# Kernel optimization log

Hardware: AMD Instinct MI355X
Metric: run time of the kernel (lower is better)

Reference implementation:

```python
import jax, jax.numpy as jnp
import numpy as np

FEAT_IN = 64     # len(nonterminals)
EMB = 256        # embedding_dim
K = 30           # sortk
B = 48           # batch items
NG = 11          # graphs per item (1 goal + 10 env)
G = B * NG       # 528 graphs
NPG = 192        # nodes per graph
EPG = 384        # edges per graph
N = G * NPG
E = G * EPG
D = 3 * EMB + 1  # 769, concat channel dim = conv5 kernel/stride
DENSE = (K // 2 - 5 + 1) * EMB  # 11*256 = 2816


def setup_inputs() -> dict:
    key = jax.random.key(0)
    ks = jax.random.split(key, 12)
    x = jax.random.normal(ks[0], (N, FEAT_IN), jnp.float32)
    # edges within each graph, no self loops (remove_self_loops in original)
    src_l = jax.random.randint(ks[1], (E,), 0, NPG)
    off = jax.random.randint(ks[2], (E,), 1, NPG)
    dst_l = (src_l + off) % NPG
    goff = (jnp.arange(E) // EPG) * NPG
    src = (src_l + goff).astype(jnp.int32)
    dst = (dst_l + goff).astype(jnp.int32)

    def lin(k, fi, fo):
        return (jax.random.normal(k, (fi, fo), jnp.float32) / np.float32(np.sqrt(fi)))

    return dict(
        x=x, src=src, dst=dst,
        W1=lin(ks[3], FEAT_IN, EMB), b1=jnp.zeros((EMB,), jnp.float32),
        W2=lin(ks[4], EMB, EMB), b2=jnp.zeros((EMB,), jnp.float32),
        W3=lin(ks[5], EMB, EMB), b3=jnp.zeros((EMB,), jnp.float32),
        W4=lin(ks[6], EMB, 1), b4=jnp.zeros((1,), jnp.float32),
        w5=jax.random.normal(ks[7], (EMB // 2, 1, D), jnp.float32) / np.float32(np.sqrt(D)),
        bc5=jnp.zeros((EMB // 2,), jnp.float32),
        w6=jax.random.normal(ks[8], (EMB, EMB // 2, 5), jnp.float32) / np.float32(np.sqrt(5 * EMB // 2)),
        bc6=jnp.zeros((EMB,), jnp.float32),
        Wc1=lin(ks[9], NG * DENSE, EMB), bc1=jnp.zeros((EMB,), jnp.float32),
        Wc2=lin(ks[10], EMB, 10), bc2=jnp.zeros((10,), jnp.float32),
    )


def _gcn(x, W, b, src, dst):
    # PyG GCNConv: add self loops, symmetric norm D^-1/2 (A+I) D^-1/2 (XW) + b
    h = x @ W
    deg = jnp.ones((N,), h.dtype).at[dst].add(1.0)  # +1 for self loop
    dis = jax.lax.rsqrt(deg)
    msg = h[src] * (dis[src] * dis[dst])[:, None]
    agg = jnp.zeros_like(h).at[dst].add(msg)
    return agg + h * (dis * dis)[:, None] + b  # self-loop norm = 1/deg


def _conv1d(x, w, b, stride):
    y = jax.lax.conv_general_dilated(x, w, (stride,), 'VALID',
                                     dimension_numbers=('NCH', 'OIH', 'NCH'))
    return y + b[None, :, None]


def reference(x, src, dst, W1, b1, W2, b2, W3, b3, W4, b4,
              w5, bc5, w6, bc6, Wc1, bc1, Wc2, bc2):
    x1 = jnp.tanh(_gcn(x, W1, b1, src, dst))
    x2 = jnp.tanh(_gcn(x1, W2, b2, src, dst))
    x3 = jnp.tanh(_gcn(x2, W3, b3, src, dst))
    x4 = jnp.tanh(_gcn(x3, W4, b4, src, dst))
    xc = jnp.concatenate([x1, x2, x3, x4], axis=-1)  # [N, D]
    xg = xc.reshape(G, NPG, D)
    # global_sort_pool: sort nodes per graph by last channel (desc), take top K
    _, idx = jax.lax.top_k(xg[:, :, -1], K)          # [G, K]
    xs = jnp.take_along_axis(xg, idx[:, :, None], axis=1)  # [G, K, D]
    seq = xs.reshape(G, 1, K * D)
    y = jax.nn.relu(_conv1d(seq, w5, bc5, D))        # [G, EMB/2, K]
    y = y.reshape(G, EMB // 2, K // 2, 2).max(axis=-1)  # MaxPool1d(2,2)
    y = jax.nn.relu(_conv1d(y, w6, bc6, 1))          # [G, EMB, K//2-4]
    emb = y.reshape(B, NG * DENSE)                   # 11 graphs per item, flattened
    h = jax.nn.relu(emb @ Wc1 + bc1)
    logits = h @ Wc2 + bc2                           # dropout is identity at eval
    return logits
```

## Files before the change

kernel.cpp:

```cpp
#include <hip/hip_runtime.h>
#include <hip/hip_bf16.h>

#define EMB   256
#define KSORT 30
#define BATCH 48
#define NGPI  11
#define GG    528
#define NPG   192
#define EPG   384
#define DCH   769
#define GC    528
#define MC    (GC*NPG)
#define EC    (GC*EPG)
#define FQ    44
#define FCH   (2816/FQ)
#define KB5   5

__device__ __forceinline__ int clampi(int v, int lo, int hi) {
  return v < lo ? lo : (v > hi ? hi : v);
}

__device__ __attribute__((aligned(16))) float g_c1[MC * EMB];
__device__ __attribute__((aligned(16))) float g_c2[MC * EMB];
__device__ __attribute__((aligned(16))) float g_c3[MC * EMB];
__device__ __attribute__((aligned(16))) float g_tb[MC * EMB];
__device__ __attribute__((aligned(16))) float g_dis[MC];
__device__ __attribute__((aligned(16))) float g_s4[MC];
__device__ __attribute__((aligned(16))) float g_x4[MC];
__device__ __attribute__((aligned(16))) int   g_indptr[MC + 1];
__device__ __attribute__((aligned(16))) int   g_ssrc[EC];
__device__ __attribute__((aligned(16))) int   g_idx[GC * KSORT];
__device__ __attribute__((aligned(16))) float g_w5t[DCH * 128];
__device__ __attribute__((aligned(16))) float g_w6t[640 * 256];
__device__ __attribute__((aligned(16))) float g_y[GC * 128 * 30];
__device__ __attribute__((aligned(16))) float g_z[GG * 2816];
__device__ __attribute__((aligned(16))) float g_hp[NGPI * FQ * BATCH * 256];
__device__ __attribute__((aligned(16))) float g_h[BATCH * 256];

__device__ __forceinline__ float* selbuf(int s) {
  return s == 0 ? g_c1 : (s == 1 ? g_c2 : g_c3);
}

__global__ __launch_bounds__(192) void build_csr_k(const int* __restrict__ src,
    const int* __restrict__ dst, int g0) {
  __shared__ int cnt[NPG];
  __shared__ int offs[NPG];
  int g = blockIdx.x, t = threadIdx.x;
  int gg = g0 + g;
  cnt[t] = 0;
  __syncthreads();
  int ebase = gg * EPG, gnb = gg * NPG, lnb = g * NPG;
  for (int e = t; e < EPG; e += 192) {
    int dl = clampi(dst[ebase + e] - gnb, 0, NPG - 1);
    atomicAdd(&cnt[dl], 1);
  }
  __syncthreads();
  if (t == 0) {
    int run = g * EPG;
    for (int i = 0; i < NPG; i++) { offs[i] = run; run += cnt[i]; }
  }
  __syncthreads();
  g_indptr[lnb + t] = offs[t];
  g_dis[lnb + t] = 1.0f / sqrtf(1.0f + (float)cnt[t]);
  if (g == 0 && t == 0) g_indptr[MC] = EC;
  __syncthreads();
  for (int e = t; e < EPG; e += 192) {
    int ee = ebase + e;
    int dl = clampi(dst[ee] - gnb, 0, NPG - 1);
    int pos = clampi(atomicAdd(&offs[dl], 1), 0, EC - 1);
    g_ssrc[pos] = clampi(src[ee] - gnb, 0, NPG - 1) + lnb;
  }
}

template<bool AX>
__global__ __launch_bounds__(256) void gemm_k(const float* __restrict__ Ax,
    int asel, const float* __restrict__ W, int Kd) {
  __shared__ float As[16 * 192];
  __shared__ float Bs[16][68];
  const int m0 = blockIdx.x * 128, n0 = blockIdx.y * 128;
  const int t = threadIdx.x;
  const int tx = t & 15, ty = t >> 4;
  const int arow = t >> 1, acol = (t & 1) * 8;
  const int awr = (arow >> 3) * 12 + (arow & 7);
  const int brow = t >> 4, bcol = tx * 4;
  float acc[8][8];
#pragma unroll
  for (int i = 0; i < 8; i++)
#pragma unroll
    for (int j = 0; j < 8; j++) acc[i][j] = 0.f;
  const float* Ap = AX ? Ax : selbuf(asel);
  const float* arp = Ap + (size_t)(m0 + arow) * Kd + acol;
  const float* bsp = W + (size_t)brow * EMB + n0 + bcol;
  const float* Wg = W + n0 + 64 + tx * 4;
  const int nt = Kd >> 4;
  float4 pa0 = *(const float4*)(arp);
  float4 pa1 = *(const float4*)(arp + 4);
  float4 pb  = *(const float4*)(bsp);
  for (int it = 0; it < nt; ++it) {
    As[(acol + 0) * 192 + awr] = pa0.x;
    As[(acol + 1) * 192 + awr] = pa0.y;
    As[(acol + 2) * 192 + awr] = pa0.z;
    As[(acol + 3) * 192 + awr] = pa0.w;
    As[(acol + 4) * 192 + awr] = pa1.x;
    As[(acol + 5) * 192 + awr] = pa1.y;
    As[(acol + 6) * 192 + awr] = pa1.z;
    As[(acol + 7) * 192 + awr] = pa1.w;
    *(float4*)&Bs[brow][bcol] = pb;
    __syncthreads();
    if (it + 1 < nt) {
      const float* ap = arp + (it + 1) * 16;
      pa0 = *(const float4*)(ap);
      pa1 = *(const float4*)(ap + 4);
      pb  = *(const float4*)(bsp + (size_t)(it + 1) * 16 * EMB);
    }
    const float* Wk = Wg + (size_t)(it * 16) * EMB;
#pragma unroll
    for (int kk = 0; kk < 16; kk++) {
      float a[8], b[8];
      *(float4*)&a[0] = *(const float4*)&As[kk * 192 + ty * 12];
      *(float4*)&a[4] = *(const float4*)&As[kk * 192 + ty * 12 + 4];
      *(float4*)&b[0] = *(const float4*)&Bs[kk][bcol];
      *(float4*)&b[4] = *(const float4*)(Wk + kk * EMB);
#pragma unroll
      for (int i = 0; i < 8; i++)
#pragma unroll
        for (int j = 0; j < 8; j++) acc[i][j] += a[i] * b[j];
    }
    __syncthreads();
  }
#pragma unroll
  for (int i = 0; i < 8; i++) {
    float* cp = g_tb + (size_t)(m0 + ty * 8 + i) * EMB + n0 + tx * 4;
    *(float4*)cp = make_float4(acc[i][0], acc[i][1], acc[i][2], acc[i][3]);
    *(float4*)(cp + 64) = make_float4(acc[i][4], acc[i][5], acc[i][6], acc[i][7]);
  }
}

__global__ __launch_bounds__(256) void agg_k(int osel,
    const float* __restrict__ bias, const float* __restrict__ W4) {
  int nb = (blockIdx.x & 7) * (MC / 4 / 8) + (blockIdx.x >> 3);
  int n = nb * 4 + (threadIdx.x >> 6);
  int lane = threadIdx.x & 63;
  float dn = g_dis[n];
  const float4* H4 = (const float4*)g_tb;
  float4 hv = H4[(size_t)n * 64 + lane];
  float sc = dn * dn;
  float ax = hv.x * sc, ay = hv.y * sc, az = hv.z * sc, aw = hv.w * sc;
  int beg = g_indptr[n], end = g_indptr[n + 1];
  for (int j = beg; j < end; j++) {
    int s = g_ssrc[j];
    float c = g_dis[s] * dn;
    float4 v = H4[(size_t)s * 64 + lane];
    ax += v.x * c; ay += v.y * c; az += v.z * c; aw += v.w * c;
  }
  float4 bv = ((const float4*)bias)[lane];
  float4 o;
  o.x = tanhf(ax + bv.x);
  o.y = tanhf(ay + bv.y);
  o.z = tanhf(az + bv.z);
  o.w = tanhf(aw + bv.w);
  ((float4*)selbuf(osel))[(size_t)n * 64 + lane] = o;
  if (W4) {
    float4 w = ((const float4*)W4)[lane];
    float s = o.x * w.x + o.y * w.y + o.z * w.z + o.w * w.w;
    for (int off = 32; off > 0; off >>= 1) s += __shfl_down(s, off, 64);
    if (lane == 0) g_s4[n] = s;
  }
}

__global__ __launch_bounds__(256) void tail1_k(const float* __restrict__ b4) {
  __shared__ float x4v[NPG];
  __shared__ float sv[256];
  __shared__ int si[256];
  const int g = blockIdx.x, t = threadIdx.x;
  const int gbase = g * NPG;
  if (t < NPG) {
    int n = gbase + t;
    float dn = g_dis[n];
    float acc = g_s4[n] * dn * dn;
    int beg = g_indptr[n], end = g_indptr[n + 1];
    for (int j = beg; j < end; j++) {
      int s = g_ssrc[j];
      acc += g_s4[s] * g_dis[s] * dn;
    }
    float v = tanhf(acc + b4[0]);
    x4v[t] = v;
    g_x4[n] = v;
  }
  __syncthreads();
  if (t < NPG) { sv[t] = x4v[t]; si[t] = t; }
  else { sv[t] = -1e30f; si[t] = 1 << 20; }
  __syncthreads();
  for (int k = 2; k <= 256; k <<= 1) {
    for (int j = k >> 1; j > 0; j >>= 1) {
      int ixj = t ^ j;
      if (ixj > t) {
        float v1 = sv[t], v2 = sv[ixj];
        int i1 = si[t], i2 = si[ixj];
        bool before_t = (v1 > v2) || (v1 == v2 && i1 < i2);
        bool up = ((t & k) == 0);
        if (up ? !before_t : before_t) {
          sv[t] = v2; sv[ixj] = v1;
          si[t] = i2; si[ixj] = i1;
        }
      }
      __syncthreads();
    }
  }
  if (t < KSORT) g_idx[g * KSORT + t] = clampi(gbase + si[t], 0, MC - 1);
}

__global__ __launch_bounds__(256) void tw5_k(const float* __restrict__ w5) {
  int i = blockIdx.x * 256 + threadIdx.x;
  if (i >= 128 * DCH) return;
  int o = i / DCH, d = i % DCH;
  g_w5t[d * 128 + o] = w5[i];
}
__global__ __launch_bounds__(256) void tw6_k(const float* __restrict__ w6) {
  int i = blockIdx.x * 256 + threadIdx.x;
  if (i >= 256 * 640) return;
  int o = i / 640, ir = i % 640;
  g_w6t[ir * 256 + o] = w6[i];
}

__global__ __launch_bounds__(128) void conv5_k(const float* __restrict__ bc5) {
  __shared__ float ar[KB5][772];
  int g = blockIdx.x, kb = blockIdx.y * KB5;
  int t = threadIdx.x;
  for (int kk = 0; kk < KB5; kk++) {
    int n = clampi(g_idx[g * KSORT + kb + kk], 0, MC - 1);
    const float* p1 = g_c1 + (size_t)n * EMB;
    const float* p2 = g_c2 + (size_t)n * EMB;
    const float* p3 = g_c3 + (size_t)n * EMB;
    for (int d = t; d < EMB; d += 128) {
      ar[kk][d] = p1[d];
      ar[kk][EMB + d] = p2[d];
      ar[kk][2 * EMB + d] = p3[d];
    }
    if (t == 0) ar[kk][768] = g_x4[n];
  }
  __syncthreads();
  float acc[KB5];
  float bias = bc5[t];
#pragma unroll
  for (int kk = 0; kk < KB5; kk++) acc[kk] = bias;
  const float* wbase = g_w5t + t;
  int d = 0;
  for (; d + 8 <= DCH; d += 8) {
    float w0 = wbase[(d + 0) * 128], w1 = wbase[(d + 1) * 128];
    float w2 = wbase[(d + 2) * 128], w3 = wbase[(d + 3) * 128];
    float w4 = wbase[(d + 4) * 128], w5 = wbase[(d + 5) * 128];
    float w6 = wbase[(d + 6) * 128], w7 = wbase[(d + 7) * 128];
#pragma unroll
    for (int kk = 0; kk < KB5; kk++) {
      float4 a0 = *(const float4*)&ar[kk][d];
      float4 a1 = *(const float4*)&ar[kk][d + 4];
      acc[kk] += a0.x * w0 + a0.y * w1 + a0.z * w2 + a0.w * w3 +
                 a1.x * w4 + a1.y * w5 + a1.z * w6 + a1.w * w7;
    }
  }
  for (; d < DCH; d++) {
    float wv = wbase[d * 128];
#pragma unroll
    for (int kk = 0; kk < KB5; kk++) acc[kk] += ar[kk][d] * wv;
  }
#pragma unroll
  for (int kk = 0; kk < KB5; kk++)
    g_y[(size_t)g * 3840 + t * KSORT + kb + kk] = fmaxf(acc[kk], 0.f);
}

__global__ __launch_bounds__(256) void conv6_k(const float* __restrict__ bc6,
                                               int g0) {
  __shared__ float s[128 * 16];
  int g = blockIdx.x, t = threadIdx.x;
  for (int i = t; i < 1920; i += 256) {
    int ch = i / 15, j = i % 15;
    const float* yp = g_y + (size_t)g * 3840 + ch * 30 + 2 * j;
    s[ch * 16 + j] = fmaxf(yp[0], yp[1]);
  }
  __syncthreads();
  float acc[11];
  float bias = bc6[t];
#pragma unroll
  for (int q = 0; q < 11; q++) acc[q] = bias;
  for (int i = 0; i < 128; i += 2) {
    float wA[5], wB[5];
#pragma unroll
    for (int r = 0; r < 5; r++) {
      wA[r] = g_w6t[(i * 5 + r) * 256 + t];
      wB[r] = g_w6t[((i + 1) * 5 + r) * 256 + t];
    }
    const float* sA = &s[i * 16];
    const float* sB = &s[(i + 1) * 16];
#pragma unroll
    for (int r = 0; r < 5; r++)
#pragma unroll
      for (int q = 0; q < 11; q++)
        acc[q] += sA[r + q] * wA[r] + sB[r + q] * wB[r];
  }
#pragma unroll
  for (int q = 0; q < 11; q++)
    g_z[(size_t)(g0 + g) * 2816 + t * 11 + q] = fmaxf(acc[q], 0.f);
}

__global__ __launch_bounds__(128) void dense1_k(const float* __restrict__ Wc1) {
  __shared__ float zs[BATCH][FCH];
  int gi = blockIdx.x;
  int obase = blockIdx.y * 128;
  int fq = blockIdx.z, f0 = fq * FCH;
  int t = threadIdx.x;
  for (int i = t; i < BATCH * FCH; i += 128) {
    int gl = i >> 6, f = i & 63;
    zs[gl][f] = g_z[(size_t)(gl * NGPI + gi) * 2816 + f0 + f];
  }
  __syncthreads();
  const float* wp = Wc1 + (size_t)gi * 2816 * 256 + (size_t)f0 * 256 + obase + t;
  float acc[BATCH];
#pragma unroll
  for (int gl = 0; gl < BATCH; gl++) acc[gl] = 0.f;
  float wc[8];
#pragma unroll
  for (int r = 0; r < 8; r++) wc[r] = wp[(size_t)r * 256];
  for (int f = 0; f < FCH; f += 8) {
    float wn[8];
    int fn = (f + 8 < FCH) ? f + 8 : f;
#pragma unroll
    for (int r = 0; r < 8; r++) wn[r] = wp[(size_t)(fn + r) * 256];
#pragma unroll
    for (int gl = 0; gl < BATCH; gl++) {
      float4 z0 = *(const float4*)&zs[gl][f];
      float4 z1 = *(const float4*)&zs[gl][f + 4];
      acc[gl] += z0.x * wc[0] + z0.y * wc[1] + z0.z * wc[2] + z0.w * wc[3] +
                 z1.x * wc[4] + z1.y * wc[5] + z1.z * wc[6] + z1.w * wc[7];
    }
#pragma unroll
    for (int r = 0; r < 8; r++) wc[r] = wn[r];
  }
  float* hp = g_hp + (size_t)(gi * FQ + fq) * (BATCH * 256);
#pragma unroll
  for (int gl = 0; gl < BATCH; gl++)
    hp[gl * 256 + obase + t] = acc[gl];
}

__global__ __launch_bounds__(256) void reduce_k() {
  int j = blockIdx.x * 256 + threadIdx.x;
  if (j >= BATCH * 256) return;
  float s0 = 0.f, s1 = 0.f, s2 = 0.f, s3 = 0.f;
  const size_t STR = BATCH * 256;
  for (int p = 0; p < NGPI * FQ; p += 4) {
    s0 += g_hp[(size_t)(p + 0) * STR + j];
    s1 += g_hp[(size_t)(p + 1) * STR + j];
    s2 += g_hp[(size_t)(p + 2) * STR + j];
    s3 += g_hp[(size_t)(p + 3) * STR + j];
  }
  g_h[j] = (s0 + s1) + (s2 + s3);
}

__global__ __launch_bounds__(256) void dense2_k(const float* __restrict__ bc1,
    const float* __restrict__ Wc2, const float* __restrict__ bc2,
    float* __restrict__ out) {
  __shared__ float hs[BATCH * 256];
  int t = threadIdx.x;
  for (int i = t; i < BATCH * 256; i += 256) {
    int o = i & 255;
    hs[i] = fmaxf(g_h[i] + bc1[o], 0.f);
  }
  __syncthreads();
  for (int i = t; i < 480; i += 256) {
    int b = i / 10, c = i % 10;
    float acc = bc2[c];
    for (int k = 0; k < 256; k++) acc += hs[b * 256 + k] * Wc2[k * 10 + c];
    out[i] = acc;
  }
}

__global__ void diag_k(float* __restrict__ out, float v) {
  int i = blockIdx.x * 256 + threadIdx.x;
  if (i < 480) out[i] = v;
}

extern "C" void kernel_launch(void* const* d_in, const int* in_sizes, int n_in,
                              void* d_out, int out_size, void* d_ws, size_t ws_size,
                              hipStream_t stream) {
  const float* x   = (const float*)d_in[0];
  const int*   src = (const int*)d_in[1];
  const int*   dst = (const int*)d_in[2];
  const float* W1  = (const float*)d_in[3];
  const float* b1  = (const float*)d_in[4];
  const float* W2  = (const float*)d_in[5];
  const float* b2  = (const float*)d_in[6];
  const float* W3  = (const float*)d_in[7];
  const float* b3  = (const float*)d_in[8];
  const float* W4  = (const float*)d_in[9];
  const float* b4  = (const float*)d_in[10];
  const float* w5  = (const float*)d_in[11];
  const float* bc5 = (const float*)d_in[12];
  const float* w6  = (const float*)d_in[13];
  const float* bc6 = (const float*)d_in[14];
  const float* Wc1 = (const float*)d_in[15];
  const float* bc1 = (const float*)d_in[16];
  const float* Wc2 = (const float*)d_in[17];
  const float* bc2 = (const float*)d_in[18];
  float* out = (float*)d_out;

  (void)hipGetLastError();
  int lcount = 0, fidx = -1;
  hipError_t ferr = hipSuccess;
  auto ck = [&]() {
    hipError_t e = hipGetLastError();
    if (e != hipSuccess && ferr == hipSuccess) { ferr = e; fidx = lcount; }
    lcount++;
  };

  tw5_k<<<(128 * DCH + 255) / 256, 256, 0, stream>>>(w5); ck();
  tw6_k<<<(256 * 640 + 255) / 256, 256, 0, stream>>>(w6); ck();

  dim3 gg(MC / 128, 2);
  build_csr_k<<<GC, 192, 0, stream>>>(src, dst, 0); ck();
  gemm_k<true><<<gg, 256, 0, stream>>>(x, 0, W1, 64); ck();
  agg_k<<<MC / 4, 256, 0, stream>>>(0, b1, nullptr); ck();
  gemm_k<false><<<gg, 256, 0, stream>>>(nullptr, 0, W2, EMB); ck();
  agg_k<<<MC / 4, 256, 0, stream>>>(1, b2, nullptr); ck();
  gemm_k<false><<<gg, 256, 0, stream>>>(nullptr, 1, W3, EMB); ck();
  agg_k<<<MC / 4, 256, 0, stream>>>(2, b3, W4); ck();
  tail1_k<<<GC, 256, 0, stream>>>(b4); ck();
  conv5_k<<<dim3(GC, 6), 128, 0, stream>>>(bc5); ck();
  conv6_k<<<GC, 256, 0, stream>>>(bc6, 0); ck();

  dense1_k<<<dim3(NGPI, 2, FQ), 128, 0, stream>>>(Wc1); ck();
  reduce_k<<<(BATCH * 256 + 255) / 256, 256, 0, stream>>>(); ck();
  dense2_k<<<1, 256, 0, stream>>>(bc1, Wc2, bc2, out); ck();

  if (ferr != hipSuccess) {
    int code = (int)ferr; if (code > 100) code = 100;
    float v = (fidx == 0) ? (1024.f + 8.f * code) : (2048.f + 16.f * code);
    diag_k<<<2, 256, 0, stream>>>(out, v);
  }
}
```

Before: 938.0 us.

## Fuse GCN GEMM and neighbor aggregation per graph using shared-memory tile

```diff
diff --git a/kernel.cpp b/kernel.cpp
--- a/kernel.cpp
+++ b/kernel.cpp
@@ -23,7 +23,6 @@
 __device__ __attribute__((aligned(16))) float g_c1[MC * EMB];
 __device__ __attribute__((aligned(16))) float g_c2[MC * EMB];
 __device__ __attribute__((aligned(16))) float g_c3[MC * EMB];
-__device__ __attribute__((aligned(16))) float g_tb[MC * EMB];
 __device__ __attribute__((aligned(16))) float g_dis[MC];
 __device__ __attribute__((aligned(16))) float g_s4[MC];
 __device__ __attribute__((aligned(16))) float g_x4[MC];
@@ -73,54 +72,61 @@
 }
 
 template<bool AX>
-__global__ __launch_bounds__(256) void gemm_k(const float* __restrict__ Ax,
-    int asel, const float* __restrict__ W, int Kd) {
-  __shared__ float As[16 * 192];
-  __shared__ float Bs[16][68];
-  const int m0 = blockIdx.x * 128, n0 = blockIdx.y * 128;
+__global__ __launch_bounds__(192) void gcn_k(const float* __restrict__ Ax,
+    int asel, int osel, const float* __restrict__ W,
+    const float* __restrict__ bias, int Kd) {
+  __shared__ float lds[13056];
+  const int bx = blockIdx.x;
+  const int g = (bx & 7) * 66 + (bx >> 5);
+  const int cb = (bx >> 3) & 3;
   const int t = threadIdx.x;
-  const int tx = t & 15, ty = t >> 4;
-  const int arow = t >> 1, acol = (t & 1) * 8;
-  const int awr = (arow >> 3) * 12 + (arow & 7);
-  const int brow = t >> 4, bcol = tx * 4;
+  const int tx = t & 7, ty = t >> 3;
+  const int n0 = cb * 64;
+  const int base = g * NPG;
   float acc[8][8];
 #pragma unroll
   for (int i = 0; i < 8; i++)
 #pragma unroll
     for (int j = 0; j < 8; j++) acc[i][j] = 0.f;
-  const float* Ap = AX ? Ax : selbuf(asel);
-  const float* arp = Ap + (size_t)(m0 + arow) * Kd + acol;
-  const float* bsp = W + (size_t)brow * EMB + n0 + bcol;
-  const float* Wg = W + n0 + 64 + tx * 4;
+  const float* Ap = (AX ? Ax : selbuf(asel)) + (size_t)base * Kd;
+  const float* arp = Ap + (size_t)t * Kd;
+  const int brow = t >> 3;
+  const float* bsp = W + (size_t)brow * EMB + n0 + tx * 8;
+  float* Bs = lds + 3072;
   const int nt = Kd >> 4;
   float4 pa0 = *(const float4*)(arp);
   float4 pa1 = *(const float4*)(arp + 4);
-  float4 pb  = *(const float4*)(bsp);
+  float4 pa2 = *(const float4*)(arp + 8);
+  float4 pa3 = *(const float4*)(arp + 12);
+  float4 pb;
+  if (t < 128) pb = *(const float4*)(bsp);
   for (int it = 0; it < nt; ++it) {
-    As[(acol + 0) * 192 + awr] = pa0.x;
-    As[(acol + 1) * 192 + awr] = pa0.y;
-    As[(acol + 2) * 192 + awr] = pa0.z;
-    As[(acol + 3) * 192 + awr] = pa0.w;
-    As[(acol + 4) * 192 + awr] = pa1.x;
-    As[(acol + 5) * 192 + awr] = pa1.y;
-    As[(acol + 6) * 192 + awr] = pa1.z;
-    As[(acol + 7) * 192 + awr] = pa1.w;
-    *(float4*)&Bs[brow][bcol] = pb;
+    lds[ 0 * 192 + t] = pa0.x; lds[ 1 * 192 + t] = pa0.y;
+    lds[ 2 * 192 + t] = pa0.z; lds[ 3 * 192 + t] = pa0.w;
+    lds[ 4 * 192 + t] = pa1.x; lds[ 5 * 192 + t] = pa1.y;
+    lds[ 6 * 192 + t] = pa1.z; lds[ 7 * 192 + t] = pa1.w;
+    lds[ 8 * 192 + t] = pa2.x; lds[ 9 * 192 + t] = pa2.y;
+    lds[10 * 192 + t] = pa2.z; lds[11 * 192 + t] = pa2.w;
+    lds[12 * 192 + t] = pa3.x; lds[13 * 192 + t] = pa3.y;
+    lds[14 * 192 + t] = pa3.z; lds[15 * 192 + t] = pa3.w;
+    if (t < 128) *(float4*)&Bs[brow * 36 + tx * 4] = pb;
     __syncthreads();
     if (it + 1 < nt) {
       const float* ap = arp + (it + 1) * 16;
       pa0 = *(const float4*)(ap);
       pa1 = *(const float4*)(ap + 4);
-      pb  = *(const float4*)(bsp + (size_t)(it + 1) * 16 * EMB);
-    }
-    const float* Wk = Wg + (size_t)(it * 16) * EMB;
+      pa2 = *(const float4*)(ap + 8);
+      pa3 = *(const float4*)(ap + 12);
+      if (t < 128) pb = *(const float4*)(bsp + (size_t)(it + 1) * 16 * EMB);
+    }
+    const float* Wk = W + (size_t)(it * 16) * EMB + n0 + tx * 8 + 4;
 #pragma unroll
     for (int kk = 0; kk < 16; kk++) {
       float a[8], b[8];
-      *(float4*)&a[0] = *(const float4*)&As[kk * 192 + ty * 12];
-      *(float4*)&a[4] = *(const float4*)&As[kk * 192 + ty * 12 + 4];
-      *(float4*)&b[0] = *(const float4*)&Bs[kk][bcol];
-      *(float4*)&b[4] = *(const float4*)(Wk + kk * EMB);
+      *(float4*)&a[0] = *(const float4*)&lds[kk * 192 + ty * 8];
+      *(float4*)&a[4] = *(const float4*)&lds[kk * 192 + ty * 8 + 4];
+      *(float4*)&b[0] = *(const float4*)&Bs[kk * 36 + tx * 4];
+      *(float4*)&b[4] = *(const float4*)(Wk + (size_t)kk * EMB);
 #pragma unroll
       for (int i = 0; i < 8; i++)
 #pragma unroll
@@ -130,42 +136,53 @@
   }
 #pragma unroll
   for (int i = 0; i < 8; i++) {
-    float* cp = g_tb + (size_t)(m0 + ty * 8 + i) * EMB + n0 + tx * 4;
-    *(float4*)cp = make_float4(acc[i][0], acc[i][1], acc[i][2], acc[i][3]);
-    *(float4*)(cp + 64) = make_float4(acc[i][4], acc[i][5], acc[i][6], acc[i][7]);
-  }
-}
-
-__global__ __launch_bounds__(256) void agg_k(int osel,
-    const float* __restrict__ bias, const float* __restrict__ W4) {
-  int nb = (blockIdx.x & 7) * (MC / 4 / 8) + (blockIdx.x >> 3);
-  int n = nb * 4 + (threadIdx.x >> 6);
+    float* hp = &lds[(ty * 8 + i) * 68 + tx * 8];
+    *(float4*)hp = make_float4(acc[i][0], acc[i][1], acc[i][2], acc[i][3]);
+    *(float4*)(hp + 4) = make_float4(acc[i][4], acc[i][5], acc[i][6], acc[i][7]);
+  }
+  __syncthreads();
+  const int n = base + t;
+  const float dn = g_dis[n];
+  const float sc = dn * dn;
+  float4 agv[16];
+#pragma unroll
+  for (int q = 0; q < 16; q++) {
+    float4 v = *(const float4*)&lds[t * 68 + q * 4];
+    agv[q] = make_float4(v.x * sc, v.y * sc, v.z * sc, v.w * sc);
+  }
+  const int beg = g_indptr[n], end = g_indptr[n + 1];
+  for (int e = beg; e < end; e++) {
+    int s = clampi(g_ssrc[e] - base, 0, NPG - 1);
+    float c = g_dis[base + s] * dn;
+#pragma unroll
+    for (int q = 0; q < 16; q++) {
+      float4 v = *(const float4*)&lds[s * 68 + q * 4];
+      agv[q].x += v.x * c; agv[q].y += v.y * c;
+      agv[q].z += v.z * c; agv[q].w += v.w * c;
+    }
+  }
+  float* outp = selbuf(osel) + (size_t)n * EMB + n0;
+  const float4* bv4 = (const float4*)bias + cb * 16;
+#pragma unroll
+  for (int q = 0; q < 16; q++) {
+    float4 bv = bv4[q];
+    float4 o;
+    o.x = tanhf(agv[q].x + bv.x);
+    o.y = tanhf(agv[q].y + bv.y);
+    o.z = tanhf(agv[q].z + bv.z);
+    o.w = tanhf(agv[q].w + bv.w);
+    *(float4*)(outp + q * 4) = o;
+  }
+}
+
+__global__ __launch_bounds__(256) void gemm4_k(const float* __restrict__ W4) {
+  int n = blockIdx.x * 4 + (threadIdx.x >> 6);
   int lane = threadIdx.x & 63;
-  float dn = g_dis[n];
-  const float4* H4 = (const float4*)g_tb;
-  float4 hv = H4[(size_t)n * 64 + lane];
-  float sc = dn * dn;
-  float ax = hv.x * sc, ay = hv.y * sc, az = hv.z * sc, aw = hv.w * sc;
-  int beg = g_indptr[n], end = g_indptr[n + 1];
-  for (int j = beg; j < end; j++) {
-    int s = g_ssrc[j];
-    float c = g_dis[s] * dn;
-    float4 v = H4[(size_t)s * 64 + lane];
-    ax += v.x * c; ay += v.y * c; az += v.z * c; aw += v.w * c;
-  }
-  float4 bv = ((const float4*)bias)[lane];
-  float4 o;
-  o.x = tanhf(ax + bv.x);
-  o.y = tanhf(ay + bv.y);
-  o.z = tanhf(az + bv.z);
-  o.w = tanhf(aw + bv.w);
-  ((float4*)selbuf(osel))[(size_t)n * 64 + lane] = o;
-  if (W4) {
-    float4 w = ((const float4*)W4)[lane];
-    float s = o.x * w.x + o.y * w.y + o.z * w.z + o.w * w.w;
-    for (int off = 32; off > 0; off >>= 1) s += __shfl_down(s, off, 64);
-    if (lane == 0) g_s4[n] = s;
-  }
+  float4 a = *(const float4*)(g_c3 + (size_t)n * EMB + lane * 4);
+  float4 w = *(const float4*)(W4 + lane * 4);
+  float s = a.x * w.x + a.y * w.y + a.z * w.z + a.w * w.w;
+  for (int off = 32; off > 0; off >>= 1) s += __shfl_down(s, off, 64);
+  if (lane == 0) g_s4[n] = s;
 }
 
 __global__ __launch_bounds__(256) void tail1_k(const float* __restrict__ b4) {
@@ -415,14 +432,11 @@
   tw5_k<<<(128 * DCH + 255) / 256, 256, 0, stream>>>(w5); ck();
   tw6_k<<<(256 * 640 + 255) / 256, 256, 0, stream>>>(w6); ck();
 
-  dim3 gg(MC / 128, 2);
   build_csr_k<<<GC, 192, 0, stream>>>(src, dst, 0); ck();
-  gemm_k<true><<<gg, 256, 0, stream>>>(x, 0, W1, 64); ck();
-  agg_k<<<MC / 4, 256, 0, stream>>>(0, b1, nullptr); ck();
-  gemm_k<false><<<gg, 256, 0, stream>>>(nullptr, 0, W2, EMB); ck();
-  agg_k<<<MC / 4, 256, 0, stream>>>(1, b2, nullptr); ck();
-  gemm_k<false><<<gg, 256, 0, stream>>>(nullptr, 1, W3, EMB); ck();
-  agg_k<<<MC / 4, 256, 0, stream>>>(2, b3, W4); ck();
+  gcn_k<true><<<GC * 4, 192, 0, stream>>>(x, 0, 0, W1, b1, 64); ck();
+  gcn_k<false><<<GC * 4, 192, 0, stream>>>(nullptr, 0, 1, W2, b2, EMB); ck();
+  gcn_k<false><<<GC * 4, 192, 0, stream>>>(nullptr, 1, 2, W3, b3, EMB); ck();
+  gemm4_k<<<MC / 4, 256, 0, stream>>>(W4); ck();
   tail1_k<<<GC, 256, 0, stream>>>(b4); ck();
   conv5_k<<<dim3(GC, 6), 128, 0, stream>>>(bc5); ck();
   conv6_k<<<GC, 256, 0, stream>>>(bc6, 0); ck();
```

Result: slower. 1.224 ms (+30.4%).
